# Optimization experiments

Hardware: AMD Instinct MI355X
Metric: run time of the kernel (lower is better)

## Reference

```python
import jax, jax.numpy as jnp
import numpy as np

IN_FEATURES = 5000
N0, N1, N2 = 512, 512, 256   # num_nodes; encoder: in->N0->N2 (skips N1), decoder: N2->N1->N0->2*in
NUM_TREATMENTS = 20
BATCH = 8192
TREAT_COLS = 2


def _glorot(key, shape):
    fan_in, fan_out = shape[-2], shape[-1]
    lim = np.sqrt(6.0 / (fan_in + fan_out)).astype(np.float32)
    return jax.random.uniform(key, shape, jnp.float32, -lim, lim)


def setup_inputs() -> dict:
    key = jax.random.key(0)
    ks = jax.random.split(key, 12)
    inp = {
        "input": jax.random.normal(ks[0], (BATCH, IN_FEATURES), jnp.float32),
        "treatment": jax.random.randint(ks[1], (BATCH, TREAT_COLS), 0, NUM_TREATMENTS + 1),
        # encoder: in -> N0 -> N2 (both layers ReLU)
        "enc_W1": _glorot(ks[2], (IN_FEATURES, N0)),
        "enc_b1": jnp.zeros((N0,), jnp.float32),
        "enc_W2": _glorot(ks[3], (N0, N2)),
        "enc_b2": jnp.zeros((N2,), jnp.float32),
        # per-treatment single layers: N2 -> N2, ReLU
        "T_W": _glorot(ks[4], (NUM_TREATMENTS, N2, N2)),
        "T_b": jnp.zeros((NUM_TREATMENTS, N2), jnp.float32),
        # decoder: N2 -> N1 -> N0 -> 2*in (last layer linear)
        "dec_W1": _glorot(ks[5], (N2, N1)),
        "dec_b1": jnp.zeros((N1,), jnp.float32),
        "dec_W2": _glorot(ks[6], (N1, N0)),
        "dec_b2": jnp.zeros((N0,), jnp.float32),
        "dec_W3": _glorot(ks[7], (N0, 2 * IN_FEATURES)),
        "dec_b3": jnp.zeros((2 * IN_FEATURES,), jnp.float32),
    }
    return inp


def reference(input, treatment, enc_W1, enc_b1, enc_W2, enc_b2, T_W, T_b,
              dec_W1, dec_b1, dec_W2, dec_b2, dec_W3, dec_b3):
    dim = input.shape[1]
    # encoder
    h = jax.nn.relu(input @ enc_W1 + enc_b1)
    embedding = jax.nn.relu(h @ enc_W2 + enc_b2)            # [B, N2]

    # per-treatment dispatch, vectorized over experts
    tvals = jnp.arange(1, NUM_TREATMENTS + 1)               # treatments are 1-indexed
    mask = jnp.any(treatment[None, :, :] == tvals[:, None, None], axis=-1)  # [T, B] bool
    # original skips a treatment unless more than one sample is assigned to it
    apply_t = jnp.sum(mask, axis=1) > 1                     # [T]
    gate = (mask & apply_t[:, None]).astype(embedding.dtype)  # [T, B]

    expert_out = jax.nn.relu(jnp.einsum('bd,tde->tbe', embedding, T_W) + T_b[:, None, :])  # [T, B, N2]
    latent_rep = jnp.einsum('tbe,tb->be', expert_out, gate)  # scatter-add of masked experts

    # decoder
    h = jax.nn.relu(latent_rep @ dec_W1 + dec_b1)
    h = jax.nn.relu(h @ dec_W2 + dec_b2)
    rec = h @ dec_W3 + dec_b3                               # [B, 2*dim]

    gene_means = rec[:, :dim]
    gene_vars = jax.nn.softplus(rec[:, dim:]) + 0.001
    return jnp.concatenate([gene_means, gene_vars], axis=1)
```

## Files before the change

kernel.cpp:

```cpp
#include <hip/hip_runtime.h>
#include <hip/hip_bf16.h>
#include <hip/hip_fp16.h>
#include <math.h>

#define BATCH 8192
#define IN_F 5000
#define KP1 5024
#define NN0 512
#define NN1 512
#define NN2 256
#define NTREAT 20
#define OUTF (2*IN_F)
#define NP3 10240

typedef _Float16 f16;
typedef _Float16 f16x8 __attribute__((ext_vector_type(8)));
typedef float f32x4 __attribute__((ext_vector_type(4)));
typedef __attribute__((address_space(3))) void as3_void;
typedef const __attribute__((address_space(1))) void cas1_void;

__device__ __forceinline__ int fswz(int row) { return (row >> 1) & 3; }

__device__ __forceinline__ float softplusf(float x) {
    return fmaxf(x, 0.f) + log1pf(expf(-fabsf(x)));
}

__global__ void zero64_kernel(int* __restrict__ p) {
    if (threadIdx.x < 64) p[threadIdx.x] = 0;
}
__global__ void count_kernel(const int* __restrict__ treat, int* __restrict__ cnt) {
    int b = blockIdx.x * blockDim.x + threadIdx.x;
    if (b >= BATCH) return;
    int t0 = treat[2*b], t1 = treat[2*b+1];
    if (t0 >= 1 && t0 <= NTREAT) atomicAdd(&cnt[t0], 1);
    if (t1 >= 1 && t1 <= NTREAT && t1 != t0) atomicAdd(&cnt[t1], 1);
}
__global__ void pair_kernel(const int* __restrict__ treat, const int* __restrict__ cnt,
                            int* __restrict__ epair) {
    int b = blockIdx.x * blockDim.x + threadIdx.x;
    if (b >= BATCH) return;
    int t0 = treat[2*b], t1 = treat[2*b+1];
    int e0 = (t0 >= 1 && t0 <= NTREAT && cnt[t0] > 1) ? (t0 - 1) : -1;
    int e1 = (t1 >= 1 && t1 <= NTREAT && t1 != t0 && cnt[t1] > 1) ? (t1 - 1) : -1;
    epair[2*b] = e0;
    epair[2*b+1] = e1;
}
__global__ void scatter_kernel(const int* __restrict__ epair, int* __restrict__ pos,
                               int* __restrict__ rows) {
    int b = blockIdx.x * blockDim.x + threadIdx.x;
    if (b >= BATCH) return;
    #pragma unroll
    for (int p = 0; p < 2; ++p) {
        int t = epair[2*b + p];
        if (t >= 0) {
            int x = atomicAdd(&pos[t], 1);
            rows[t * BATCH + x] = b * 2 + p;
        }
    }
}

__global__ __launch_bounds__(256) void convw_kernel(
    const float* __restrict__ W, f16* __restrict__ Whi, f16* __restrict__ Wlo,
    int K, int N, int Kp) {
    __shared__ float t[64][65];
    const int k0 = blockIdx.x * 64;
    const int n0 = blockIdx.y * 64;
    const int tid = threadIdx.x;
    #pragma unroll
    for (int i = 0; i < 16; ++i) {
        int idx = tid + i*256;
        int r = idx >> 6, c = idx & 63;
        float v = 0.f;
        if (k0 + r < K && n0 + c < N) v = W[(size_t)(k0+r)*N + n0 + c];
        t[r][c] = v;
    }
    __syncthreads();
    const int n = tid >> 2;
    const int q0 = (tid & 3) * 2;
    const int f = fswz(n0 + n);
    #pragma unroll
    for (int h = 0; h < 2; ++h) {
        int q = q0 + h;
        if (k0 + q*8 >= Kp) continue;
        f16x8 hv, lv;
        #pragma unroll
        for (int j = 0; j < 8; ++j) {
            float x = t[q*8 + j][n];
            f16 hi = (f16)x;
            hv[j] = hi;
            lv[j] = (f16)(x - (float)hi);
        }
        size_t base = (size_t)(n0 + n) * Kp + (size_t)(k0 + (((q & 3) ^ f) << 3) + (q >> 2) * 32);
        *(f16x8*)&Whi[base] = hv;
        *(f16x8*)&Wlo[base] = lv;
    }
}

__global__ __launch_bounds__(256) void expert_gemm(
    const float* __restrict__ emb, const float* __restrict__ T_W,
    const float* __restrict__ T_b, const int* __restrict__ pos,
    const int* __restrict__ rows, float* __restrict__ latA, float* __restrict__ latB) {
    const int t = blockIdx.x;
    const int n = pos[t];
    const int base = blockIdx.y * 16;
    if (base >= n) return;
    const int nr = min(16, n - base);
    __shared__ float se[16][256];
    __shared__ int ridx[16];
    const int tid = threadIdx.x;
    if (tid < 16) ridx[tid] = (tid < nr) ? rows[t * BATCH + base + tid] : 0;
    __syncthreads();
    #pragma unroll
    for (int s = 0; s < 16; ++s)
        se[s][tid] = (s < nr) ? emb[(size_t)(ridx[s] >> 1) * NN2 + tid] : 0.f;
    __syncthreads();
    float acc[16];
    const float bcol = T_b[t * NN2 + tid];
    #pragma unroll
    for (int s = 0; s < 16; ++s) acc[s] = bcol;
    const float* W = T_W + (size_t)t * NN2 * NN2 + tid;
    for (int d0 = 0; d0 < NN2; d0 += 4) {
        float w0 = W[(size_t)(d0+0) * NN2];
        float w1 = W[(size_t)(d0+1) * NN2];
        float w2 = W[(size_t)(d0+2) * NN2];
        float w3 = W[(size_t)(d0+3) * NN2];
        #pragma unroll
        for (int s = 0; s < 16; ++s) {
            float4 e = *(const float4*)&se[s][d0];
            acc[s] = fmaf(e.x, w0, fmaf(e.y, w1, fmaf(e.z, w2, fmaf(e.w, w3, acc[s]))));
        }
    }
    for (int s = 0; s < nr; ++s) {
        int rp = ridx[s];
        float* dst = (rp & 1) ? latB : latA;
        dst[(size_t)(rp >> 1) * NN2 + tid] = fmaxf(acc[s], 0.f);
    }
}

__global__ __launch_bounds__(256) void latconv_kernel(
    const float* __restrict__ latA, const float* __restrict__ latB,
    f16* __restrict__ lhi, f16* __restrict__ llo) {
    const int idx = blockIdx.x * 256 + threadIdx.x;
    const int m = idx >> 8, k = idx & 255;
    float v = latA[idx] + latB[idx];
    f16 hi = (f16)v;
    size_t o = (size_t)m * NN2 + (size_t)(k ^ (fswz(m) << 3));
    lhi[o] = hi;
    llo[o] = (f16)(v - (float)hi);
}

template<int MODE, bool XCVT, int BN, int BM = 256>
__global__ __launch_bounds__((BM == 128) ? 256 : 512, 2) void gemm8(
    const f16* __restrict__ Xhi, const f16* __restrict__ Xlo,
    const float* __restrict__ X32, int ldx,
    const f16* __restrict__ Whi, const f16* __restrict__ Wlo,
    const float* __restrict__ bias,
    float* __restrict__ C32, f16* __restrict__ Chi, f16* __restrict__ Clo,
    int Kp, int K_real, int N_real, int NpOut, int halfN) {
    constexpr int NTH = (BM == 128) ? 256 : 512;
    constexpr int NWAVE = NTH / 64;
    constexpr int WN_WAVES = (BN == 256) ? 4 : 2;
    constexpr int WM_WAVES = NWAVE / WN_WAVES;
    constexpr int WMT = BM / WM_WAVES;
    constexpr int WNT = BN / WN_WAVES;
    constexpr int MF = WMT / 16;
    constexpr int NF = WNT / 16;
    constexpr int XSZ = BM * 32;
    constexpr int WSZ = BN * 32;
    constexpr int GLL = (BN == 64) ? 5 : 8;
    __shared__ f16 lds[2][2*XSZ + 2*WSZ];

    const int tid = threadIdx.x;
    const int wid = tid >> 6;
    const int lane = tid & 63;
    const int lr = lane & 15;
    const int ls = lane >> 4;
    const int m0 = blockIdx.y * BM;
    const int n0 = blockIdx.x * BN;
    const int wm = (wid / WN_WAVES) * WMT;
    const int wn = (wid % WN_WAVES) * WNT;
    const int koff = ((ls ^ ((lr >> 1) & 3)) << 3);
    const int nk = Kp / 32;

    f32x4 acc[MF][NF] = {};

    auto stage = [&](int bi, int kt) {
        f16* Xh = lds[bi];
        f16* Xl = Xh + XSZ;
        f16* Wh = Xl + XSZ;
        f16* Wl = Wh + WSZ;
        const int kk = kt * 32 + (lane & 3) * 8;
        const int rlo = lane >> 2;
        if constexpr (BN == 128) {
            #pragma unroll
            for (int c = 0; c < 2; ++c) {
                const int rb = wid * 32 + c * 16;
                const size_t g = (size_t)(n0 + rb + rlo) * Kp + kk;
                __builtin_amdgcn_global_load_lds((cas1_void*)(Whi + g), (as3_void*)(Wh + rb*32), 16, 0, 0);
                __builtin_amdgcn_global_load_lds((cas1_void*)(Wlo + g), (as3_void*)(Wl + rb*32), 16, 0, 0);
            }
        } else {
            const int rb = (wid & 3) * 16;
            const size_t g = (size_t)(n0 + rb + rlo) * Kp + kk;
            const f16* src = (wid < 4) ? (Whi + g) : (Wlo + g);
            f16* dst = ((wid < 4) ? Wh : Wl) + rb*32;
            __builtin_amdgcn_global_load_lds((cas1_void*)src, (as3_void*)dst, 16, 0, 0);
        }
        if constexpr (!XCVT) {
            if constexpr (BM == 256) {
                #pragma unroll
                for (int c = 0; c < 2; ++c) {
                    const int rb = c * 128 + wid * 16;
                    const size_t g = (size_t)(m0 + rb + rlo) * Kp + kk;
                    __builtin_amdgcn_global_load_lds((cas1_void*)(Xhi + g), (as3_void*)(Xh + rb*32), 16, 0, 0);
                    __builtin_amdgcn_global_load_lds((cas1_void*)(Xlo + g), (as3_void*)(Xl + rb*32), 16, 0, 0);
                }
            } else {
                #pragma unroll
                for (int c = 0; c < 2; ++c) {
                    const int rb = wid * 32 + c * 16;
                    const size_t g = (size_t)(m0 + rb + rlo) * Kp + kk;
                    __builtin_amdgcn_global_load_lds((cas1_void*)(Xhi + g), (as3_void*)(Xh + rb*32), 16, 0, 0);
                    __builtin_amdgcn_global_load_lds((cas1_void*)(Xlo + g), (as3_void*)(Xl + rb*32), 16, 0, 0);
                }
            }
        } else {
            const int ar = tid >> 1;
            const int q0 = (tid & 1) * 2;
            const int fr = fswz(ar);
            const int k0 = kt * 32;
            const float* ap = X32 + (size_t)(m0 + ar) * ldx + (size_t)(k0 + q0 * 8);
            float v[16];
            if (k0 + 32 <= K_real) {
                float4 u0 = *(const float4*)(ap);
                float4 u1 = *(const float4*)(ap + 4);
                float4 u2 = *(const float4*)(ap + 8);
                float4 u3 = *(const float4*)(ap + 12);
                v[0]=u0.x; v[1]=u0.y; v[2]=u0.z; v[3]=u0.w;
                v[4]=u1.x; v[5]=u1.y; v[6]=u1.z; v[7]=u1.w;
                v[8]=u2.x; v[9]=u2.y; v[10]=u2.z; v[11]=u2.w;
                v[12]=u3.x; v[13]=u3.y; v[14]=u3.z; v[15]=u3.w;
            } else {
                #pragma unroll
                for (int j2 = 0; j2 < 16; ++j2) {
                    int kk2 = k0 + q0*8 + j2;
                    v[j2] = (kk2 < K_real) ? X32[(size_t)(m0 + ar) * ldx + kk2] : 0.f;
                }
            }
            #pragma unroll
            for (int h2 = 0; h2 < 2; ++h2) {
                f16x8 hv, lv;
                #pragma unroll
                for (int j2 = 0; j2 < 8; ++j2) {
                    float x = v[h2*8 + j2];
                    f16 hh = (f16)x;
                    hv[j2] = hh;
                    lv[j2] = (f16)(x - (float)hh);
                }
                const int dst = ar*32 + (((q0 + h2) ^ fr) << 3);
                *(f16x8*)&Xh[dst] = hv;
                *(f16x8*)&Xl[dst] = lv;
            }
        }
    };

    if constexpr (!XCVT) {
        stage(0, 0);
        stage(1, 1);
        for (int t = 0; t < nk; ++t) {
            if (t + 1 < nk) {
                asm volatile("s_waitcnt vmcnt(%0)" :: "i"(GLL) : "memory");
            } else {
                asm volatile("s_waitcnt vmcnt(0)" ::: "memory");
            }
            __builtin_amdgcn_s_barrier();
            const f16* Xh = lds[t & 1];
            const f16* Xl = Xh + XSZ;
            const f16* Wh = Xl + XSZ;
            const f16* Wl = Wh + WSZ;
            f16x8 bh[NF], bl[NF], ah[MF], al[MF];
            #pragma unroll
            for (int j = 0; j < NF; ++j) {
                const int r = (wn + j*16 + lr) * 32 + koff;
                bh[j] = *(const f16x8*)&Wh[r];
                bl[j] = *(const f16x8*)&Wl[r];
            }
            #pragma unroll
            for (int i = 0; i < MF; ++i) {
                const int r = (wm + i*16 + lr) * 32 + koff;
                ah[i] = *(const f16x8*)&Xh[r];
                al[i] = *(const f16x8*)&Xl[r];
            }
            asm volatile("s_waitcnt lgkmcnt(0)" ::: "memory");
            __builtin_amdgcn_sched_barrier(0);
            __builtin_amdgcn_s_barrier();
            if (t + 2 < nk) stage(t & 1, t + 2);
            __builtin_amdgcn_s_setprio(1);
            #pragma unroll
            for (int i = 0; i < MF; ++i)
                #pragma unroll
                for (int j = 0; j < NF; ++j)
                    acc[i][j] = __builtin_amdgcn_mfma_f32_16x16x32_f16(ah[i], bh[j], acc[i][j], 0, 0, 0);
            #pragma unroll
            for (int i = 0; i < MF; ++i)
                #pragma unroll
                for (int j = 0; j < NF; ++j)
                    acc[i][j] = __builtin_amdgcn_mfma_f32_16x16x32_f16(ah[i], bl[j], acc[i][j], 0, 0, 0);
            #pragma unroll
            for (int i = 0; i < MF; ++i)
                #pragma unroll
                for (int j = 0; j < NF; ++j)
                    acc[i][j] = __builtin_amdgcn_mfma_f32_16x16x32_f16(al[i], bh[j], acc[i][j], 0, 0, 0);
            __builtin_amdgcn_s_setprio(0);
        }
    } else {
        stage(0, 0);
        __syncthreads();
        for (int t = 0; t < nk; ++t) {
            if (t + 1 < nk) stage((t + 1) & 1, t + 1);
            const f16* Xh = lds[t & 1];
            const f16* Xl = Xh + XSZ;
            const f16* Wh = Xl + XSZ;
            const f16* Wl = Wh + WSZ;
            f16x8 bh[NF], bl[NF];
            #pragma unroll
            for (int j = 0; j < NF; ++j) {
                const int r = (wn + j*16 + lr) * 32 + koff;
                bh[j] = *(const f16x8*)&Wh[r];
                bl[j] = *(const f16x8*)&Wl[r];
            }
            __builtin_amdgcn_s_setprio(1);
            #pragma unroll
            for (int ih = 0; ih < MF; ih += 4) {
                f16x8 ah[4], al[4];
                #pragma unroll
                for (int i = 0; i < 4; ++i) {
                    const int r = (wm + (ih + i)*16 + lr) * 32 + koff;
                    ah[i] = *(const f16x8*)&Xh[r];
                    al[i] = *(const f16x8*)&Xl[r];
                }
                #pragma unroll
                for (int i = 0; i < 4; ++i)
                    #pragma unroll
                    for (int j = 0; j < NF; ++j)
                        acc[ih+i][j] = __builtin_amdgcn_mfma_f32_16x16x32_f16(ah[i], bh[j], acc[ih+i][j], 0, 0, 0);
                #pragma unroll
                for (int i = 0; i < 4; ++i)
                    #pragma unroll
                    for (int j = 0; j < NF; ++j)
                        acc[ih+i][j] = __builtin_amdgcn_mfma_f32_16x16x32_f16(ah[i], bl[j], acc[ih+i][j], 0, 0, 0);
                #pragma unroll
                for (int i = 0; i < 4; ++i)
                    #pragma unroll
                    for (int j = 0; j < NF; ++j)
                        acc[ih+i][j] = __builtin_amdgcn_mfma_f32_16x16x32_f16(al[i], bh[j], acc[ih+i][j], 0, 0, 0);
            }
            __builtin_amdgcn_s_setprio(0);
            __syncthreads();
        }
    }

    #pragma unroll
    for (int i = 0; i < MF; ++i) {
        #pragma unroll
        for (int j = 0; j < NF; ++j) {
            const int col = n0 + wn + j*16 + lr;
            if (col >= N_real) continue;
            const float bcol = bias[col];
            #pragma unroll
            for (int q = 0; q < 4; ++q) {
                const int m = m0 + wm + i*16 + ls*4 + q;
                float vv = acc[i][j][q] + bcol;
                if (MODE == 0) {
                    C32[(size_t)m * N_real + col] = fmaxf(vv, 0.f);
                } else if (MODE == 1) {
                    vv = fmaxf(vv, 0.f);
                    f16 hi = (f16)vv;
                    const size_t idx = (size_t)m * NpOut + (size_t)(col ^ (fswz(m) << 3));
                    Chi[idx] = hi;
                    Clo[idx] = (f16)(vv - (float)hi);
                } else {
                    if (col >= halfN) vv = softplusf(vv) + 0.001f;
                    C32[(size_t)m * N_real + col] = vv;
                }
            }
        }
    }
}

__global__ __launch_bounds__(256, 3) void gemm_dec3_areg(
    const f16* __restrict__ Xhi, const f16* __restrict__ Xlo,
    const f16* __restrict__ Whi, const f16* __restrict__ Wlo,
    const float* __restrict__ bias, float* __restrict__ C32) {
    constexpr int WSZ = 128 * 32;
    __shared__ f16 lds[2][2 * WSZ];

    const int tid = threadIdx.x;
    const int wid = tid >> 6;
    const int lane = tid & 63;
    const int lr = lane & 15;
    const int ls = lane >> 4;
    const int m0 = blockIdx.y * 128;
    const int n0 = blockIdx.x * 128;
    const int wm = (wid >> 1) * 64;
    const int wn = (wid & 1) * 64;
    const int koff = ((ls ^ ((lr >> 1) & 3)) << 3);
    const int kk_s = (lane & 3) * 8;
    const int rlo = lane >> 2;

    const int f_a = (lr >> 1) & 3;
    size_t arow[4];
    #pragma unroll
    for (int i = 0; i < 4; ++i)
        arow[i] = (size_t)(m0 + wm + i*16 + lr) * NN0 + ((ls ^ f_a) << 3);

    f32x4 acc[4][4] = {};

    auto stageW = [&](int bi, int kt) {
        f16* Wh = lds[bi];
        f16* Wl = Wh + WSZ;
        const int kk = kt * 32 + kk_s;
        const int rb = wid * 32;
        #pragma unroll
        for (int c = 0; c < 2; ++c) {
            const size_t g = (size_t)(n0 + rb + c*16 + rlo) * NN0 + kk;
            __builtin_amdgcn_global_load_lds((cas1_void*)(Whi + g), (as3_void*)(Wh + (rb + c*16)*32), 16, 0, 0);
            __builtin_amdgcn_global_load_lds((cas1_void*)(Wlo + g), (as3_void*)(Wl + (rb + c*16)*32), 16, 0, 0);
        }
    };

    stageW(0, 0);
    __syncthreads();
    for (int t = 0; t < 16; ++t) {
        if (t + 1 < 16) stageW((t + 1) & 1, t + 1);
        f16x8 ah[4], al[4];
        #pragma unroll
        for (int i = 0; i < 4; ++i) {
            const size_t ga = arow[i] + t * 32;
            ah[i] = *(const f16x8*)(Xhi + ga);
            al[i] = *(const f16x8*)(Xlo + ga);
        }
        const f16* Wh = lds[t & 1];
        const f16* Wl = Wh + WSZ;
        f16x8 bh[4], bl[4];
        #pragma unroll
        for (int j = 0; j < 4; ++j) {
            const int r = (wn + j*16 + lr) * 32 + koff;
            bh[j] = *(const f16x8*)&Wh[r];
            bl[j] = *(const f16x8*)&Wl[r];
        }
        __builtin_amdgcn_s_setprio(1);
        #pragma unroll
        for (int i = 0; i < 4; ++i)
            #pragma unroll
            for (int j = 0; j < 4; ++j)
                acc[i][j] = __builtin_amdgcn_mfma_f32_16x16x32_f16(ah[i], bh[j], acc[i][j], 0, 0, 0);
        #pragma unroll
        for (int i = 0; i < 4; ++i)
            #pragma unroll
            for (int j = 0; j < 4; ++j)
                acc[i][j] = __builtin_amdgcn_mfma_f32_16x16x32_f16(ah[i], bl[j], acc[i][j], 0, 0, 0);
        #pragma unroll
        for (int i = 0; i < 4; ++i)
            #pragma unroll
            for (int j = 0; j < 4; ++j)
                acc[i][j] = __builtin_amdgcn_mfma_f32_16x16x32_f16(al[i], bh[j], acc[i][j], 0, 0, 0);
        __builtin_amdgcn_s_setprio(0);
        __syncthreads();
    }

    #pragma unroll
    for (int i = 0; i < 4; ++i) {
        #pragma unroll
        for (int j = 0; j < 4; ++j) {
            const int col = n0 + wn + j*16 + lr;
            if (col >= OUTF) continue;
            const float bcol = bias[col];
            #pragma unroll
            for (int q = 0; q < 4; ++q) {
                const int m = m0 + wm + i*16 + ls*4 + q;
                float vv = acc[i][j][q] + bcol;
                if (col >= IN_F) vv = softplusf(vv) + 0.001f;
                C32[(size_t)m * OUTF + col] = vv;
            }
        }
    }
}

extern "C" void kernel_launch(void* const* d_in, const int* in_sizes, int n_in,
                              void* d_out, int out_size, void* d_ws, size_t ws_size,
                              hipStream_t stream) {
    const float* input  = (const float*)d_in[0];
    const int*   treat  = (const int*)d_in[1];
    const float* enc_W1 = (const float*)d_in[2];
    const float* enc_b1 = (const float*)d_in[3];
    const float* enc_W2 = (const float*)d_in[4];
    const float* enc_b2 = (const float*)d_in[5];
    const float* T_W    = (const float*)d_in[6];
    const float* T_b    = (const float*)d_in[7];
    const float* dec_W1 = (const float*)d_in[8];
    const float* dec_b1 = (const float*)d_in[9];
    const float* dec_W2 = (const float*)d_in[10];
    const float* dec_b2 = (const float*)d_in[11];
    const float* dec_W3 = (const float*)d_in[12];
    const float* dec_b3 = (const float*)d_in[13];
    float* out = (float*)d_out;

    uint8_t* p = (uint8_t*)d_ws;
    f16* h1hi = (f16*)p;  float* latA = (float*)p;  p += (size_t)BATCH*NN0*2;
    f16* h1lo = (f16*)p;  float* latB = (float*)p;  p += (size_t)BATCH*NN0*2;
    float* emb = (float*)p;  f16* h4hi = (f16*)p;   p += (size_t)BATCH*NN2*4;
    f16* lathi = (f16*)p;  f16* h4lo = (f16*)p;     p += (size_t)BATCH*NN2*2;
    f16* latlo = (f16*)p;                           p += (size_t)BATCH*NN2*2;
    f16* w1hi = (f16*)p;               p += (size_t)NN0*KP1*2;
    f16* w1lo = (f16*)p;               p += (size_t)NN0*KP1*2;
    f16* w2hi = (f16*)p;               p += (size_t)NN2*NN0*2;
    f16* w2lo = (f16*)p;               p += (size_t)NN2*NN0*2;
    f16* dw1hi = (f16*)p;              p += (size_t)NN1*NN2*2;
    f16* dw1lo = (f16*)p;              p += (size_t)NN1*NN2*2;
    f16* dw2hi = (f16*)p;              p += (size_t)NN0*NN1*2;
    f16* dw2lo = (f16*)p;              p += (size_t)NN0*NN1*2;
    f16* dw3hi = (f16*)p;              p += (size_t)NP3*NN0*2;
    f16* dw3lo = (f16*)p;              p += (size_t)NP3*NN0*2;
    int* cnt   = (int*)p;              p += 32*4;
    int* pos   = (int*)p;              p += 32*4;
    int* epair = (int*)p;              p += (size_t)BATCH*2*4;
    int* rows  = (int*)p;              p += (size_t)NTREAT*BATCH*4;
    f16* h3hi = h1hi;
    f16* h3lo = h1lo;

    zero64_kernel<<<1, 64, 0, stream>>>(cnt);
    count_kernel<<<BATCH/256, 256, 0, stream>>>(treat, cnt);
    pair_kernel<<<BATCH/256, 256, 0, stream>>>(treat, cnt, epair);
    scatter_kernel<<<BATCH/256, 256, 0, stream>>>(epair, pos, rows);

    convw_kernel<<<dim3((KP1+63)/64, NN0/64), 256, 0, stream>>>(enc_W1, w1hi, w1lo, IN_F, NN0, KP1);
    convw_kernel<<<dim3(NN0/64, NN2/64), 256, 0, stream>>>(enc_W2, w2hi, w2lo, NN0, NN2, NN0);
    convw_kernel<<<dim3(NN2/64, NN1/64), 256, 0, stream>>>(dec_W1, dw1hi, dw1lo, NN2, NN1, NN2);
    convw_kernel<<<dim3(NN1/64, NN0/64), 256, 0, stream>>>(dec_W2, dw2hi, dw2lo, NN1, NN0, NN1);
    convw_kernel<<<dim3(NN0/64, NP3/64), 256, 0, stream>>>(dec_W3, dw3hi, dw3lo, NN0, OUTF, NN0);

    gemm8<1, true, 64><<<dim3(NN0/64, BATCH/256), 512, 0, stream>>>(
        nullptr, nullptr, input, IN_F, w1hi, w1lo, enc_b1,
        nullptr, h1hi, h1lo, KP1, IN_F, NN0, NN0, 0);
    gemm8<0, false, 64><<<dim3(NN2/64, BATCH/256), 512, 0, stream>>>(
        h1hi, h1lo, nullptr, 0, w2hi, w2lo, enc_b2,
        emb, nullptr, nullptr, NN0, NN0, NN2, NN2, 0);
    hipMemsetAsync(latA, 0, (size_t)BATCH*NN2*4*2, stream);
    expert_gemm<<<dim3(NTREAT, BATCH/16), 256, 0, stream>>>(emb, T_W, T_b, pos, rows, latA, latB);
    latconv_kernel<<<BATCH*NN2/256, 256, 0, stream>>>(latA, latB, lathi, latlo);
    gemm8<1, false, 64><<<dim3(NN1/64, BATCH/256), 512, 0, stream>>>(
        lathi, latlo, nullptr, 0, dw1hi, dw1lo, dec_b1,
        nullptr, h3hi, h3lo, NN2, NN2, NN1, NN1, 0);
    gemm8<1, false, 64><<<dim3(NN0/64, BATCH/256), 512, 0, stream>>>(
        h3hi, h3lo, nullptr, 0, dw2hi, dw2lo, dec_b2,
        nullptr, h4hi, h4lo, NN1, NN1, NN0, NN0, 0);
    gemm_dec3_areg<<<dim3(NP3/128, BATCH/128), 256, 0, stream>>>(
        h4hi, h4lo, dw3hi, dw3lo, dec_b3, out);
}
```

Measured before the change: 921.1 us.

## Prefetch A fragments one k-step ahead and remap dec3 blocks per XCD

New measurement: 1.303 ms. +41.5%, slower.

```diff
diff --git a/kernel.cpp b/kernel.cpp
--- a/kernel.cpp
+++ b/kernel.cpp
@@ -400,8 +400,13 @@
     const int lane = tid & 63;
     const int lr = lane & 15;
     const int ls = lane >> 4;
-    const int m0 = blockIdx.y * 128;
-    const int n0 = blockIdx.x * 128;
+    const int d = blockIdx.x + blockIdx.y * 80;
+    const int cx = d & 7;
+    const int jj = d >> 3;
+    const int mt = cx * 8 + jj / 80;
+    const int nt = jj % 80;
+    const int m0 = mt * 128;
+    const int n0 = nt * 128;
     const int wm = (wid >> 1) * 64;
     const int wn = (wid & 1) * 64;
     const int koff = ((ls ^ ((lr >> 1) & 3)) << 3);
@@ -428,17 +433,26 @@
             __builtin_amdgcn_global_load_lds((cas1_void*)(Wlo + g), (as3_void*)(Wl + (rb + c*16)*32), 16, 0, 0);
         }
     };
-
-    stageW(0, 0);
-    __syncthreads();
-    for (int t = 0; t < 16; ++t) {
-        if (t + 1 < 16) stageW((t + 1) & 1, t + 1);
-        f16x8 ah[4], al[4];
+    auto loadA = [&](int kt, f16x8 (&ah)[4], f16x8 (&al)[4]) {
         #pragma unroll
         for (int i = 0; i < 4; ++i) {
-            const size_t ga = arow[i] + t * 32;
+            const size_t ga = arow[i] + (size_t)kt * 32;
             ah[i] = *(const f16x8*)(Xhi + ga);
             al[i] = *(const f16x8*)(Xlo + ga);
+        }
+    };
+
+    f16x8 ahA[4], alA[4], ahB[4], alB[4];
+
+    stageW(0, 0);
+    loadA(0, ahA, alA);
+    __syncthreads();
+
+    auto body = [&](int t, f16x8 (&ahc)[4], f16x8 (&alc)[4],
+                    f16x8 (&ahn)[4], f16x8 (&aln)[4]) {
+        if (t + 1 < 16) {
+            stageW((t + 1) & 1, t + 1);
+            loadA(t + 1, ahn, aln);
         }
         const f16* Wh = lds[t & 1];
         const f16* Wl = Wh + WSZ;
@@ -454,19 +468,25 @@
         for (int i = 0; i < 4; ++i)
             #pragma unroll
             for (int j = 0; j < 4; ++j)
-                acc[i][j] = __builtin_amdgcn_mfma_f32_16x16x32_f16(ah[i], bh[j], acc[i][j], 0, 0, 0);
+                acc[i][j] = __builtin_amdgcn_mfma_f32_16x16x32_f16(ahc[i], bh[j], acc[i][j], 0, 0, 0);
         #pragma unroll
         for (int i = 0; i < 4; ++i)
             #pragma unroll
             for (int j = 0; j < 4; ++j)
-                acc[i][j] = __builtin_amdgcn_mfma_f32_16x16x32_f16(ah[i], bl[j], acc[i][j], 0, 0, 0);
+                acc[i][j] = __builtin_amdgcn_mfma_f32_16x16x32_f16(ahc[i], bl[j], acc[i][j], 0, 0, 0);
         #pragma unroll
         for (int i = 0; i < 4; ++i)
             #pragma unroll
             for (int j = 0; j < 4; ++j)
-                acc[i][j] = __builtin_amdgcn_mfma_f32_16x16x32_f16(al[i], bh[j], acc[i][j], 0, 0, 0);
+                acc[i][j] = __builtin_amdgcn_mfma_f32_16x16x32_f16(alc[i], bh[j], acc[i][j], 0, 0, 0);
         __builtin_amdgcn_s_setprio(0);
-        __syncthreads();
+        if (t + 1 < 16) __syncthreads();
+    };
+
+    #pragma unroll
+    for (int t = 0; t < 16; t += 2) {
+        body(t,     ahA, alA, ahB, alB);
+        body(t + 1, ahB, alB, ahA, alA);
     }
 
     #pragma unroll
```
